# Optimization experiments

Measured on AMD Instinct MI355X. Metric: run time of the kernel, lower is better.

The kernel has to match this reference:

```python
import jax, jax.numpy as jnp
import numpy as np

NUM_HEADS = 12
WINDOW = 14
GLOBAL_LAYERS = (1,)
N_LAYERS = 2
EPS = 1e-6
PATCH = 16


def layer_norm(x, w, b):
    m = x.mean(-1, keepdims=True)
    v = ((x - m) ** 2).mean(-1, keepdims=True)
    return (x - m) * jax.lax.rsqrt(v + EPS) * w + b


def layer_norm_2d(x, w, b):
    # channels_first LayerNorm over C of [B,C,H,W]
    m = x.mean(1, keepdims=True)
    v = ((x - m) ** 2).mean(1, keepdims=True)
    return (x - m) * jax.lax.rsqrt(v + EPS) * w[None, :, None, None] + b[None, :, None, None]


def get_rel_pos(size, rel_pos):
    # q_size == k_size == size and rel_pos has exactly 2*size-1 rows,
    # so F.interpolate is identity -> direct relative-coordinate lookup.
    coords = jnp.arange(size)
    idx = coords[:, None] - coords[None, :] + (size - 1)  # [size, size]
    return rel_pos[idx]  # [size, size, head_dim]


def attention(x, qkv_w, qkv_b, proj_w, proj_b, rel_h, rel_w):
    B, H, W, C = x.shape
    hd = C // NUM_HEADS
    qkv = x.reshape(B, H * W, C) @ qkv_w.T + qkv_b                       # [B,HW,3C]
    qkv = qkv.reshape(B, H * W, 3, NUM_HEADS, hd).transpose(2, 0, 3, 1, 4)
    qkv = qkv.reshape(3, B * NUM_HEADS, H * W, hd)
    q, k, v = qkv[0], qkv[1], qkv[2]
    attn = jnp.einsum('bqd,bkd->bqk', q * (hd ** -0.5), k)               # [Bn,HW,HW]
    Rh = get_rel_pos(H, rel_h)                                           # [H,H,hd]
    Rw = get_rel_pos(W, rel_w)                                           # [W,W,hd]
    qr = q.reshape(B * NUM_HEADS, H, W, hd)
    rel_h_t = jnp.einsum('bhwc,hkc->bhwk', qr, Rh)                       # [Bn,H,W,H]
    rel_w_t = jnp.einsum('bhwc,wkc->bhwk', qr, Rw)                       # [Bn,H,W,W]
    attn = attn.reshape(B * NUM_HEADS, H, W, H, W)
    attn = attn + rel_h_t[:, :, :, :, None] + rel_w_t[:, :, :, None, :]
    attn = attn.reshape(B * NUM_HEADS, H * W, H * W)
    attn = jax.nn.softmax(attn.astype(jnp.float32), axis=-1).astype(q.dtype)
    out = jnp.einsum('bqk,bkd->bqd', attn, v)
    out = out.reshape(B, NUM_HEADS, H, W, hd).transpose(0, 2, 3, 1, 4).reshape(B, H, W, C)
    return out @ proj_w.T + proj_b


def window_partition(x, ws):
    B, H, W, C = x.shape
    pad_h = (-H) % ws
    pad_w = (-W) % ws
    x = jnp.pad(x, ((0, 0), (0, pad_h), (0, pad_w), (0, 0)))
    Hp, Wp = H + pad_h, W + pad_w
    x = x.reshape(B, Hp // ws, ws, Wp // ws, ws, C).transpose(0, 1, 3, 2, 4, 5)
    return x.reshape(-1, ws, ws, C), (Hp, Wp)


def window_unpartition(win, ws, pad_hw, hw):
    Hp, Wp = pad_hw
    H, W = hw
    C = win.shape[-1]
    B = win.shape[0] // ((Hp // ws) * (Wp // ws))
    x = win.reshape(B, Hp // ws, Wp // ws, ws, ws, C).transpose(0, 1, 3, 2, 4, 5)
    return x.reshape(B, Hp, Wp, C)[:, :H, :W, :]


def _forward(pixel_values, patch_w, patch_b, pos_embed, ln1_w, ln1_b, qkv_w, qkv_b,
             proj_w, proj_b, rel_h0, rel_w0, rel_h1, rel_w1, ln2_w, ln2_b,
             mlp1_w, mlp1_b, mlp2_w, mlp2_b, neck_conv1_w, neck_ln1_w, neck_ln1_b,
             neck_conv2_w, neck_ln2_w, neck_ln2_b):
    # patch embed (16x16 stride-16 conv) -> [B,64,64,768]
    x = jax.lax.conv_general_dilated(pixel_values, patch_w, (PATCH, PATCH), 'VALID',
                                     dimension_numbers=('NCHW', 'OIHW', 'NCHW'))
    x = x.transpose(0, 2, 3, 1) + patch_b
    x = x + pos_embed
    rels = [(rel_h0, rel_w0), (rel_h1, rel_w1)]
    for i in range(N_LAYERS):
        shortcut = x
        h = layer_norm(x, ln1_w[i], ln1_b[i])
        ws = 0 if i in GLOBAL_LAYERS else WINDOW
        if ws > 0:
            H, W = h.shape[1], h.shape[2]
            h, pad_hw = window_partition(h, ws)
        h = attention(h, qkv_w[i], qkv_b[i], proj_w[i], proj_b[i], *rels[i])
        if ws > 0:
            h = window_unpartition(h, ws, pad_hw, (H, W))
        x = shortcut + h
        m = layer_norm(x, ln2_w[i], ln2_b[i])
        m = jax.nn.gelu(m @ mlp1_w[i].T + mlp1_b[i], approximate=False)
        x = x + (m @ mlp2_w[i].T + mlp2_b[i])
    # neck: 1x1 conv -> LN2d -> 3x3 conv -> LN2d (convs have no bias)
    x = x.transpose(0, 3, 1, 2)                                          # [B,C,H,W]
    x = jnp.einsum('bchw,oc->bohw', x, neck_conv1_w[:, :, 0, 0])
    x = layer_norm_2d(x, neck_ln1_w, neck_ln1_b)
    x = jax.lax.conv_general_dilated(x, neck_conv2_w, (1, 1), ((1, 1), (1, 1)),
                                     dimension_numbers=('NCHW', 'OIHW', 'NCHW'))
    x = layer_norm_2d(x, neck_ln2_w, neck_ln2_b)
    return x


def setup_inputs() -> dict:
    ks = iter(jax.random.split(jax.random.key(0), 40))

    def rn(shape, s=0.02):
        return jax.random.normal(next(ks), shape, jnp.float32) * s

    C, NL, MLP, OC = 768, N_LAYERS, 3072, 256
    return {
        'pixel_values': jax.random.normal(next(ks), (1, 3, 1024, 1024), jnp.float32),
        'patch_w': rn((C, 3, PATCH, PATCH)),
        'patch_b': rn((C,)),
        'pos_embed': rn((1, 64, 64, C)),
        'ln1_w': jnp.ones((NL, C)), 'ln1_b': jnp.zeros((NL, C)),
        'qkv_w': rn((NL, 3 * C, C)), 'qkv_b': rn((NL, 3 * C)),
        'proj_w': rn((NL, C, C)), 'proj_b': rn((NL, C)),
        'rel_h0': rn((2 * WINDOW - 1, 64)), 'rel_w0': rn((2 * WINDOW - 1, 64)),
        'rel_h1': rn((2 * 64 - 1, 64)), 'rel_w1': rn((2 * 64 - 1, 64)),
        'ln2_w': jnp.ones((NL, C)), 'ln2_b': jnp.zeros((NL, C)),
        'mlp1_w': rn((NL, MLP, C)), 'mlp1_b': rn((NL, MLP)),
        'mlp2_w': rn((NL, C, MLP)), 'mlp2_b': rn((NL, C)),
        'neck_conv1_w': rn((OC, C, 1, 1)),
        'neck_ln1_w': jnp.ones((OC,)), 'neck_ln1_b': jnp.zeros((OC,)),
        'neck_conv2_w': rn((OC, OC, 3, 3)),
        'neck_ln2_w': jnp.ones((OC,)), 'neck_ln2_b': jnp.zeros((OC,)),
    }


def reference(pixel_values, patch_w, patch_b, pos_embed, ln1_w, ln1_b, qkv_w, qkv_b,
              proj_w, proj_b, rel_h0, rel_w0, rel_h1, rel_w1, ln2_w, ln2_b,
              mlp1_w, mlp1_b, mlp2_w, mlp2_b, neck_conv1_w, neck_ln1_w, neck_ln1_b,
              neck_conv2_w, neck_ln2_w, neck_ln2_b):
    return _forward(pixel_values, patch_w, patch_b, pos_embed, ln1_w, ln1_b, qkv_w,
                    qkv_b, proj_w, proj_b, rel_h0, rel_w0, rel_h1, rel_w1, ln2_w,
                    ln2_b, mlp1_w, mlp1_b, mlp2_w, mlp2_b, neck_conv1_w, neck_ln1_w,
                    neck_ln1_b, neck_conv2_w, neck_ln2_w, neck_ln2_b)
```

## Files before the change

kernel.cpp:

```cpp
#include <hip/hip_runtime.h>
#include <hip/hip_bf16.h>
#include <cmath>
#include <cstddef>

#define THREADS 256
typedef unsigned short u16;
typedef unsigned int u32;
typedef __attribute__((ext_vector_type(8))) short bf16x8;
typedef __attribute__((ext_vector_type(4))) float f32x4;
#define MFMA16(a, b, c) __builtin_amdgcn_mfma_f32_16x16x32_bf16(a, b, c, 0, 0, 0)

__device__ __forceinline__ float bf2f(u16 u) {
  union { u32 i; float f; } x; x.i = ((u32)u) << 16; return x.f;
}
__device__ __forceinline__ u16 f2bf(float f) {
  __hip_bfloat16 h = __float2bfloat16(f);
  return *reinterpret_cast<u16*>(&h);
}
__device__ __forceinline__ u32 f2bf2(float a, float b) {
  __hip_bfloat162 h = __float22bfloat162_rn(make_float2(a, b));
  return *reinterpret_cast<u32*>(&h);
}

__device__ __forceinline__ void gload16(const u16* g, u16* l) {
  __builtin_amdgcn_global_load_lds(
      (const __attribute__((address_space(1))) unsigned int*)g,
      (__attribute__((address_space(3))) unsigned int*)l, 16, 0, 0);
}

__device__ __forceinline__ float block_reduce_sum256(float v, float* red4) {
  for (int off = 32; off > 0; off >>= 1) v += __shfl_down(v, off);
  __syncthreads();
  if ((threadIdx.x & 63) == 0) red4[threadIdx.x >> 6] = v;
  __syncthreads();
  return red4[0] + red4[1] + red4[2] + red4[3];
}

__global__ void f2b_kernel(const float* __restrict__ in, u16* __restrict__ out,
                           int n) {
  int i = (blockIdx.x * THREADS + threadIdx.x) * 4;
  if (i >= n) return;
  float4 v = *reinterpret_cast<const float4*>(in + i);
  ushort4 o;
  o.x = f2bf(v.x); o.y = f2bf(v.y); o.z = f2bf(v.z); o.w = f2bf(v.w);
  *reinterpret_cast<ushort4*>(out + i) = o;
}

__global__ void neck2w_kernel(const float* __restrict__ src,
                              u16* __restrict__ dst) {
  int idx = blockIdx.x * THREADS + threadIdx.x;
  if (idx >= 256 * 2304) return;
  int o = idx / 2304, r = idx % 2304;
  int n9 = r >> 8, c = r & 255;
  dst[idx] = f2bf(src[(size_t)(o * 256 + c) * 9 + n9]);
}

__global__ void im2col_patch_kernel(const float* __restrict__ img,
                                    u16* __restrict__ out) {
  int idx = blockIdx.x * THREADS + threadIdx.x;
  if (idx >= 4096 * 768) return;
  int col = idx % 768, tok = idx / 768;
  int ph = tok / 64, pw = tok % 64;
  int c = col / 256, r = col % 256;
  int i = r / 16, j = r % 16;
  out[idx] = f2bf(img[(size_t)(c * 1024 + ph * 16 + i) * 1024 + pw * 16 + j]);
}

template <int MODE, int BN>
__global__ __launch_bounds__(256)
void gemm_bf16(const u16* __restrict__ A, const u16* __restrict__ B,
               const float* __restrict__ bias, const float* __restrict__ res,
               void* __restrict__ out, void* __restrict__ out2,
               int M, int N, int K) {
  constexpr int NF = BN / 32;
  __shared__ __attribute__((aligned(16))) u16 As[128 * 64];
  __shared__ __attribute__((aligned(16))) u16 Bs[BN * 64];
  const int t = threadIdx.x;
  const int w = t >> 6, l = t & 63;
  const int m0 = blockIdx.y * 128, n0 = blockIdx.x * BN;
  const int wm = (w >> 1) * 64, wn = (w & 1) * (BN / 2);
  f32x4 acc[4][NF];
#pragma unroll
  for (int i = 0; i < 4; ++i)
#pragma unroll
    for (int j = 0; j < NF; ++j) acc[i][j] = (f32x4){0.f, 0.f, 0.f, 0.f};

  const int rr = l >> 3;
  const int cc = ((l & 7) ^ rr) * 8;
  const u16* aP[4];
  const u16* bP[NF];
#pragma unroll
  for (int j = 0; j < 4; ++j) {
    int ar = m0 + w * 32 + j * 8 + rr;
    if (ar >= M) ar = M - 1;
    aP[j] = A + (size_t)ar * K + cc;
  }
#pragma unroll
  for (int j = 0; j < NF; ++j)
    bP[j] = B + (size_t)(n0 + w * (BN / 4) + j * 8 + rr) * K + cc;
  u16* asw = &As[w * 2048];
  u16* bsw = &Bs[w * (BN * 16)];

  for (int k0 = 0; k0 < K; k0 += 64) {
    __syncthreads();
#pragma unroll
    for (int j = 0; j < 4; ++j) gload16(aP[j] + k0, asw + j * 512);
#pragma unroll
    for (int j = 0; j < NF; ++j) gload16(bP[j] + k0, bsw + j * 512);
    asm volatile("s_waitcnt vmcnt(0)" ::: "memory");
    __syncthreads();
#pragma unroll
    for (int kc = 0; kc < 2; ++kc) {
      bf16x8 af[4], bf[NF];
#pragma unroll
      for (int i = 0; i < 4; ++i) {
        int ar = wm + i * 16 + (l & 15);
        int ac = (kc * 4 + (l >> 4)) ^ (ar & 7);
        af[i] = *reinterpret_cast<const bf16x8*>(&As[ar * 64 + ac * 8]);
      }
#pragma unroll
      for (int j = 0; j < NF; ++j) {
        int br = wn + j * 16 + (l & 15);
        int bc = (kc * 4 + (l >> 4)) ^ (br & 7);
        bf[j] = *reinterpret_cast<const bf16x8*>(&Bs[br * 64 + bc * 8]);
      }
#pragma unroll
      for (int i = 0; i < 4; ++i)
#pragma unroll
        for (int j = 0; j < NF; ++j)
          acc[i][j] = MFMA16(af[i], bf[j], acc[i][j]);
    }
  }

#pragma unroll
  for (int i = 0; i < 4; ++i) {
#pragma unroll
    for (int reg = 0; reg < 4; ++reg) {
      int m = m0 + wm + i * 16 + (l >> 4) * 4 + reg;
      if (m >= M) continue;
#pragma unroll
      for (int j = 0; j < NF; ++j) {
        int n = n0 + wn + j * 16 + (l & 15);
        float v = acc[i][j][reg];
        if (bias) v += bias[n];
        if (MODE == 0 || MODE == 3) {
          if (res) v += res[(size_t)m * N + n];
          ((float*)out)[(size_t)m * N + n] = v;
          if (MODE == 3) ((u16*)out2)[(size_t)m * N + n] = f2bf(v);
        } else if (MODE == 1) {
          v = 0.5f * v * (1.0f + erff(v * 0.70710678118654752f));
          ((u16*)out)[(size_t)m * N + n] = f2bf(v);
        } else {
          float sc = (n < 768) ? 0.125f : 1.0f;
          ((u16*)out)[(size_t)m * N + n] = f2bf(v * sc);
        }
      }
    }
  }
}

template <int WHICH>
__global__ __launch_bounds__(256)
void relpos_mfma_kernel(const u16* __restrict__ qkvb,
                        const u16* __restrict__ Rtab,
                        u16* __restrict__ relout) {
  __shared__ __attribute__((aligned(16))) u16 Ql[64 * 64];
  __shared__ __attribute__((aligned(16))) u16 Rl[64 * 64];
  const int t = threadIdx.x, w = t >> 6, l = t & 63;
  const int head = blockIdx.x >> 6;
  const int fixed = blockIdx.x & 63;
  const int rr = l >> 3;
  const int cc = ((l & 7) ^ rr) * 8;

#pragma unroll
  for (int j = 0; j < 2; ++j) {
    int row = w * 16 + j * 8 + rr;
    int tok = (WHICH == 0) ? (fixed * 64 + row) : (row * 64 + fixed);
    gload16(qkvb + (size_t)tok * 2304 + head * 64 + cc, &Ql[w * 1024 + j * 512]);
    int rrow = fixed - row + 63;
    gload16(Rtab + rrow * 64 + cc, &Rl[w * 1024 + j * 512]);
  }
  asm volatile("s_waitcnt vmcnt(0)" ::: "memory");
  __syncthreads();

  f32x4 acc[4];
#pragma unroll
  for (int j = 0; j < 4; ++j) acc[j] = (f32x4){0.f, 0.f, 0.f, 0.f};
#pragma unroll
  for (int kc = 0; kc < 2; ++kc) {
    int ar = w * 16 + (l & 15);
    int ac = (kc * 4 + (l >> 4)) ^ (ar & 7);
    bf16x8 af = *reinterpret_cast<const bf16x8*>(&Ql[ar * 64 + ac * 8]);
#pragma unroll
    for (int j = 0; j < 4; ++j) {
      int br = j * 16 + (l & 15);
      int bc = (kc * 4 + (l >> 4)) ^ (br & 7);
      bf16x8 bf = *reinterpret_cast<const bf16x8*>(&Rl[br * 64 + bc * 8]);
      acc[j] = MFMA16(af, bf, acc[j]);
    }
  }

#pragma unroll
  for (int j = 0; j < 4; ++j) {
#pragma unroll
    for (int reg = 0; reg < 4; ++reg) {
      int m = w * 16 + (l >> 4) * 4 + reg;
      int n = j * 16 + (l & 15);
      size_t o = (WHICH == 0)
                     ? ((((size_t)head * 64 + fixed) * 64 + m) * 64 + n)
                     : ((((size_t)head * 64 + m) * 64 + fixed) * 64 + n);
      relout[o] = f2bf(acc[j][reg] * 8.0f);
    }
  }
}

__global__ void ln_row_kernel(const float* __restrict__ in,
                              const float* __restrict__ w,
                              const float* __restrict__ b,
                              u16* __restrict__ out, int D) {
  __shared__ float red[4];
  size_t base = (size_t)blockIdx.x * D;
  float s = 0.f, s2 = 0.f;
  for (int i = threadIdx.x; i < D; i += THREADS) {
    float v = in[base + i];
    s += v; s2 += v * v;
  }
  s = block_reduce_sum256(s, red);
  s2 = block_reduce_sum256(s2, red);
  float m = s / (float)D;
  float var = s2 / (float)D - m * m;
  float inv = rsqrtf(var + 1e-6f);
  for (int i = threadIdx.x; i < D; i += THREADS) {
    float v = in[base + i];
    out[base + i] = f2bf((v - m) * inv * w[i] + b[i]);
  }
}

__global__ void win_part_kernel(const u16* __restrict__ h,
                                u16* __restrict__ out) {
  int idx = blockIdx.x * THREADS + threadIdx.x;
  if (idx >= 4900 * 768) return;
  int c = idx % 768;
  int tok = idx / 768;
  int win = tok / 196, r = tok % 196;
  int wy = r / 14, wx = r % 14;
  int gy = (win / 5) * 14 + wy;
  int gx = (win % 5) * 14 + wx;
  out[idx] = (gy < 64 && gx < 64) ? h[((size_t)gy * 64 + gx) * 768 + c] : (u16)0;
}

__global__ void win_unpart_add_kernel(const float* __restrict__ p,
                                      float* __restrict__ x) {
  int idx = blockIdx.x * THREADS + threadIdx.x;
  if (idx >= 4096 * 768) return;
  int c = idx % 768;
  int tok = idx / 768;
  int gy = tok / 64, gx = tok % 64;
  int win = (gy / 14) * 5 + (gx / 14);
  int wy = gy % 14, wx = gx % 14;
  x[idx] += p[((size_t)(win * 196 + wy * 14 + wx)) * 768 + c];
}

__global__ void add_kernel(const float* __restrict__ p, float* __restrict__ x,
                           int n) {
  int idx = blockIdx.x * THREADS + threadIdx.x;
  if (idx < n) x[idx] += p[idx];
}

__global__ void relpos_kernel(const u16* __restrict__ qkvb,
                              const float* __restrict__ rh_tab,
                              const float* __restrict__ rw_tab,
                              u16* __restrict__ relh,
                              u16* __restrict__ relw,
                              int S, int total) {
  int idx = blockIdx.x * THREADS + threadIdx.x;
  if (idx >= total) return;
  int k = idx % S;
  int r = idx / S;
  int qw = r % S; r /= S;
  int qh = r % S; r /= S;
  int head = r % 12;
  int win = r / 12;
  int seq = S * S;
  int tok = win * seq + qh * S + qw;
  const u16* q = qkvb + (size_t)tok * 2304 + head * 64;
  const float* rh = rh_tab + (size_t)(qh - k + S - 1) * 64;
  const float* rw = rw_tab + (size_t)(qw - k + S - 1) * 64;
  float sh = 0.f, sw = 0.f;
#pragma unroll
  for (int d0 = 0; d0 < 64; d0 += 8) {
    uint4 qv = *reinterpret_cast<const uint4*>(q + d0);
    u16 qs[8];
    *reinterpret_cast<uint4*>(qs) = qv;
#pragma unroll
    for (int i = 0; i < 8; ++i) {
      float qq = bf2f(qs[i]);
      sh = fmaf(qq, rh[d0 + i], sh);
      sw = fmaf(qq, rw[d0 + i], sw);
    }
  }
  relh[idx] = f2bf(sh * 8.0f);
  relw[idx] = f2bf(sw * 8.0f);
}

template <int S>
__global__ __launch_bounds__(256)
void attn_mfma_kernel(const u16* __restrict__ qkvb,
                      const u16* __restrict__ RHt,
                      const u16* __restrict__ RWt,
                      u16* __restrict__ out) {
  constexpr int SEQ = S * S;
  constexpr int NKT = (SEQ + 63) / 64;
  constexpr bool DB = (S == 64);
  constexpr int BIAS_N = (S == 14) ? 320 : 1024;
  extern __shared__ __attribute__((aligned(16))) u16 smem[];
  u16* KlA[2];
  u16* VtA[2];
  u16* Plb;
  u16* RHlb;
  u16* RWlb = nullptr;
  if constexpr (DB) {
    KlA[0] = smem;          KlA[1] = smem + 4096;
    VtA[0] = smem + 8192;   VtA[1] = smem + 12288;
    Plb = smem + 16384;
    RHlb = smem + 20480;
  } else {
    KlA[0] = smem;          KlA[1] = smem;
    VtA[0] = smem + 4096;   VtA[1] = smem + 4096;
    Plb = smem + 8192;
    RHlb = smem + 12288;
    RWlb = RHlb + 4 * BIAS_N;
  }

  const int t = threadIdx.x;
  const int w = t >> 6;
  const int l = t & 63;
  const int g = l >> 4;
  const int q = l & 15;
  const int bn = blockIdx.y;
  const int win = bn / 12, head = bn % 12;
  const int qbase = blockIdx.x * 64 + w * 16;
  const size_t tokbase = (size_t)win * SEQ;
  u16* Pl = Plb + w * 1024;
  u16* RHl = RHlb + w * BIAS_N;
  u16* RWl = RWlb + w * BIAS_N;

  {
    int ql = l >> 2;
    int qglob = qbase + ql;
    if (qglob > SEQ - 1) qglob = SEQ - 1;
    int qh = qglob / S, qw = qglob - qh * S;
    size_t bh = (((size_t)bn * S + qh) * S + qw) * S;
    for (int i = l & 3; i < S; i += 4) {
      RHl[i * 16 + ql] = RHt[bh + i];
      if constexpr (S == 14) RWl[i * 16 + ql] = RWt[bh + i];
    }
  }

  float rwreg[4][4];
  if constexpr (S == 64) {
    int qglob = qbase + q;
    size_t rwb = (((size_t)bn * 64 + (qglob >> 6)) * 64 + (qglob & 63)) * 64;
#pragma unroll
    for (int sub = 0; sub < 4; ++sub)
#pragma unroll
      for (int reg = 0; reg < 4; ++reg)
        rwreg[sub][reg] = bf2f(RWt[rwb + sub * 16 + g * 4 + reg]);
  }

  bf16x8 qf[2];
  {
    int qglob = qbase + q;
    if (qglob > SEQ - 1) qglob = SEQ - 1;
    const u16* qp = qkvb + (tokbase + qglob) * 2304 + head * 64 + g * 8;
    qf[0] = *reinterpret_cast<const bf16x8*>(qp);
    qf[1] = *reinterpret_cast<const bf16x8*>(qp + 32);
  }

  float m_run = -1e30f, l_run = 0.f;
  f32x4 Oacc[4];
#pragma unroll
  for (int dn = 0; dn < 4; ++dn) Oacc[dn] = (f32x4){0.f, 0.f, 0.f, 0.f};

  const int rr = l >> 3;
  const int kcc = ((l & 7) ^ rr) * 8;
  const int vkey = t & 63, vdg = t >> 6;

  auto stageK = [&](int kt, u16* Kd) {
#pragma unroll
    for (int j = 0; j < 2; ++j) {
      int kk = kt * 64 + w * 16 + j * 8 + rr;
      if (kk > SEQ - 1) kk = SEQ - 1;
      gload16(qkvb + (tokbase + kk) * 2304 + 768 + head * 64 + kcc,
              &Kd[w * 1024 + j * 512]);
    }
  };
  auto loadV = [&](int kt, uint4& a, uint4& b) {
    int kk = kt * 64 + vkey;
    if (kk > SEQ - 1) kk = SEQ - 1;
    const uint4* src = reinterpret_cast<const uint4*>(
        qkvb + (tokbase + kk) * 2304 + 1536 + head * 64 + vdg * 16);
    a = src[0];
    b = src[1];
  };
  auto writeV = [&](uint4 a, uint4 b, u16* Vd) {
    u16 arr[16];
    *reinterpret_cast<uint4*>(&arr[0]) = a;
    *reinterpret_cast<uint4*>(&arr[8]) = b;
#pragma unroll
    for (int i = 0; i < 16; ++i)
      Vd[(vdg * 16 + i) * 64 + (vkey ^ ((i & 7) << 3))] = arr[i];
  };

  auto computeTile = [&](int kt, u16* Kl, u16* Vt) {
    const int k0 = kt * 64;
    f32x4 Sacc[4];
#pragma unroll
    for (int sub = 0; sub < 4; ++sub) {
      Sacc[sub] = (f32x4){0.f, 0.f, 0.f, 0.f};
#pragma unroll
      for (int kc = 0; kc < 2; ++kc) {
        int key = sub * 16 + q;
        int chunk = (kc * 4 + g) ^ (key & 7);
        bf16x8 kfr = *reinterpret_cast<const bf16x8*>(&Kl[key * 64 + (chunk << 3)]);
        Sacc[sub] = MFMA16(kfr, qf[kc], Sacc[sub]);
      }
    }

    float sv[4][4];
    float tmax = -1e30f;
    if constexpr (S == 64) {
      float rhv = bf2f(RHl[kt * 16 + q]);
#pragma unroll
      for (int sub = 0; sub < 4; ++sub)
#pragma unroll
        for (int reg = 0; reg < 4; ++reg) {
          float s = Sacc[sub][reg] + rhv + rwreg[sub][reg];
          sv[sub][reg] = s;
          tmax = fmaxf(tmax, s);
        }
    } else {
#pragma unroll
      for (int sub = 0; sub < 4; ++sub)
#pragma unroll
        for (int reg = 0; reg < 4; ++reg) {
          int key = k0 + sub * 16 + g * 4 + reg;
          float s = -1e30f;
          if (key < SEQ) {
            int kh = key / S, kw = key - kh * S;
            s = Sacc[sub][reg] + bf2f(RHl[kh * 16 + q]) + bf2f(RWl[kw * 16 + q]);
          }
          sv[sub][reg] = s;
          tmax = fmaxf(tmax, s);
        }
    }
    tmax = fmaxf(tmax, __shfl_xor(tmax, 16));
    tmax = fmaxf(tmax, __shfl_xor(tmax, 32));

    if (!__all(tmax - m_run <= 8.0f)) {
      float mn = fmaxf(m_run, tmax);
      float sc = __expf(m_run - mn);
      l_run *= sc;
      m_run = mn;
#pragma unroll
      for (int reg = 0; reg < 4; ++reg) {
        float scq = __shfl(sc, g * 4 + reg);
#pragma unroll
        for (int dn = 0; dn < 4; ++dn) Oacc[dn][reg] *= scq;
      }
    }

    float psum = 0.f;
#pragma unroll
    for (int sub = 0; sub < 4; ++sub)
#pragma unroll
      for (int pr = 0; pr < 2; ++pr) {
        float p0 = __expf(sv[sub][2 * pr] - m_run);
        float p1 = __expf(sv[sub][2 * pr + 1] - m_run);
        psum += p0 + p1;
        u32 pk = f2bf2(p0, p1);
        int idx = (q * 64 + sub * 16 + g * 4 + pr * 2) ^ ((q & 7) << 3);
        *reinterpret_cast<u32*>(&Pl[idx]) = pk;
      }
    psum += __shfl_xor(psum, 16);
    psum += __shfl_xor(psum, 32);
    l_run += psum;

#pragma unroll
    for (int kc = 0; kc < 2; ++kc) {
      int chunk = (kc * 4 + g) ^ (q & 7);
      bf16x8 pa = *reinterpret_cast<const bf16x8*>(&Pl[q * 64 + (chunk << 3)]);
#pragma unroll
      for (int dn = 0; dn < 4; ++dn) {
        bf16x8 vb = *reinterpret_cast<const bf16x8*>(
            &Vt[(dn * 16 + q) * 64 + (chunk << 3)]);
        Oacc[dn] = MFMA16(pa, vb, Oacc[dn]);
      }
    }
  };

  if constexpr (DB) {
    uint4 va, vb0;
    stageK(0, KlA[0]);
    loadV(0, va, vb0);
    asm volatile("s_waitcnt vmcnt(0)" ::: "memory");
    writeV(va, vb0, VtA[0]);
    __syncthreads();
    for (int kt = 0; kt < NKT; ++kt) {
      const int cur = kt & 1;
      const bool pf = (kt + 1 < NKT);
      if (pf) {
        stageK(kt + 1, KlA[cur ^ 1]);
        loadV(kt + 1, va, vb0);
      }
      computeTile(kt, KlA[cur], VtA[cur]);
      if (pf) {
        asm volatile("s_waitcnt vmcnt(0)" ::: "memory");
        writeV(va, vb0, VtA[cur ^ 1]);
      }
      __syncthreads();
    }
  } else {
    for (int kt = 0; kt < NKT; ++kt) {
      __syncthreads();
      stageK(kt, KlA[0]);
      uint4 va, vb0;
      loadV(kt, va, vb0);
      writeV(va, vb0, VtA[0]);
      asm volatile("s_waitcnt vmcnt(0)" ::: "memory");
      __syncthreads();
      computeTile(kt, KlA[0], VtA[0]);
    }
  }

  float invq = 1.0f / l_run;
#pragma unroll
  for (int reg = 0; reg < 4; ++reg) {
    int ql = g * 4 + reg;
    int qglob = qbase + ql;
    if (qglob >= SEQ) continue;
    float inv = __shfl(invq, ql);
    u16* op = out + (tokbase + qglob) * 768 + head * 64;
#pragma unroll
    for (int dn = 0; dn < 4; ++dn)
      op[dn * 16 + q] = f2bf(Oacc[dn][reg] * inv);
  }
}

__global__ void neck_im2col_kernel(const u16* __restrict__ ln,
                                   u16* __restrict__ out) {
  int idx = blockIdx.x * THREADS + threadIdx.x;
  if (idx >= 4096 * 2304) return;
  int col = idx % 2304, tok = idx / 2304;
  int n9 = col >> 8, c = col & 255;
  int y = tok >> 6, x = tok & 63;
  int yy = y + n9 / 3 - 1, xx = x + n9 % 3 - 1;
  out[idx] = (yy >= 0 && yy < 64 && xx >= 0 && xx < 64)
                 ? ln[((size_t)yy * 64 + xx) * 256 + c]
                 : (u16)0;
}

__global__ void ln2d_out_kernel(const float* __restrict__ in,
                                const float* __restrict__ w,
                                const float* __restrict__ b,
                                float* __restrict__ out) {
  __shared__ float red[4];
  int tok = blockIdx.x, t = threadIdx.x;
  float v = in[(size_t)tok * 256 + t];
  float s = block_reduce_sum256(v, red);
  float m = s / 256.f;
  float dv = v - m;
  float s2 = block_reduce_sum256(dv * dv, red);
  float inv = rsqrtf(s2 / 256.f + 1e-6f);
  out[(size_t)t * 4096 + tok] = dv * inv * w[t] + b[t];
}

extern "C" void kernel_launch(void* const* d_in, const int* in_sizes, int n_in,
                              void* d_out, int out_size, void* d_ws,
                              size_t ws_size, hipStream_t stream) {
  const float* pixel_values = (const float*)d_in[0];
  const float* patch_w = (const float*)d_in[1];
  const float* patch_b = (const float*)d_in[2];
  const float* pos_embed = (const float*)d_in[3];
  const float* ln1_w = (const float*)d_in[4];
  const float* ln1_b = (const float*)d_in[5];
  const float* qkv_w = (const float*)d_in[6];
  const float* qkv_b = (const float*)d_in[7];
  const float* proj_w = (const float*)d_in[8];
  const float* proj_b = (const float*)d_in[9];
  const float* rel_h0 = (const float*)d_in[10];
  const float* rel_w0 = (const float*)d_in[11];
  const float* rel_h1 = (const float*)d_in[12];
  const float* rel_w1 = (const float*)d_in[13];
  const float* ln2_w = (const float*)d_in[14];
  const float* ln2_b = (const float*)d_in[15];
  const float* mlp1_w = (const float*)d_in[16];
  const float* mlp1_b = (const float*)d_in[17];
  const float* mlp2_w = (const float*)d_in[18];
  const float* mlp2_b = (const float*)d_in[19];
  const float* neck1_w = (const float*)d_in[20];
  const float* nln1_w = (const float*)d_in[21];
  const float* nln1_b = (const float*)d_in[22];
  const float* neck2_w = (const float*)d_in[23];
  const float* nln2_w = (const float*)d_in[24];
  const float* nln2_b = (const float*)d_in[25];
  float* out = (float*)d_out;

  float* X = (float*)d_ws;
  u16* Xb = (u16*)(X + 3145728);
  float* H = (float*)(Xb + 3145728);
  u16* Ab1 = (u16*)(H + 3763200);
  u16* Ab2 = Ab1 + 3763200;
  u16* QKVb = Ab2 + 12582912;
  u16* RHb = QKVb + 11289600;
  u16* RWb = RHb + 3145728;
  u16* AOb = RWb + 3145728;
  u16* Wb = AOb + 3763200;
  u16* RTb = Wb + 2359296;
  u16* RTb2 = RTb + 8128;
  u16* LNb = Ab2 + 11520000;

#define CVT(src, n) f2b_kernel<<<((n) / 4 + THREADS - 1) / THREADS, THREADS, 0, stream>>>(src, Wb, n)

  im2col_patch_kernel<<<12288, THREADS, 0, stream>>>(pixel_values, Ab2);
  CVT(patch_w, 589824);
  gemm_bf16<0, 64><<<dim3(12, 32), THREADS, 0, stream>>>(
      Ab2, Wb, patch_b, pos_embed, X, nullptr, 4096, 768, 768);

  ln_row_kernel<<<4096, THREADS, 0, stream>>>(X, ln1_w, ln1_b, Ab2, 768);
  win_part_kernel<<<14700, THREADS, 0, stream>>>(Ab2, Ab1);
  CVT(qkv_w, 1769472);
  gemm_bf16<2, 128><<<dim3(18, 39), THREADS, 0, stream>>>(
      Ab1, Wb, qkv_b, nullptr, QKVb, nullptr, 4900, 2304, 768);
  {
    int total = 25 * 12 * 14 * 14 * 14;
    relpos_kernel<<<(total + THREADS - 1) / THREADS, THREADS, 0, stream>>>(
        QKVb, rel_h0, rel_w0, RHb, RWb, 14, total);
  }
  attn_mfma_kernel<14><<<dim3(4, 300), THREADS, 29696, stream>>>(QKVb, RHb, RWb, AOb);
  CVT(proj_w, 589824);
  gemm_bf16<0, 64><<<dim3(12, 39), THREADS, 0, stream>>>(
      AOb, Wb, proj_b, nullptr, H, nullptr, 4900, 768, 768);
  win_unpart_add_kernel<<<12288, THREADS, 0, stream>>>(H, X);
  ln_row_kernel<<<4096, THREADS, 0, stream>>>(X, ln2_w, ln2_b, Ab1, 768);
  CVT(mlp1_w, 2359296);
  gemm_bf16<1, 128><<<dim3(24, 32), THREADS, 0, stream>>>(
      Ab1, Wb, mlp1_b, nullptr, Ab2, nullptr, 4096, 3072, 768);
  CVT(mlp2_w, 2359296);
  gemm_bf16<0, 64><<<dim3(12, 32), THREADS, 0, stream>>>(
      Ab2, Wb, mlp2_b, X, X, nullptr, 4096, 768, 3072);

  ln_row_kernel<<<4096, THREADS, 0, stream>>>(X, ln1_w + 768, ln1_b + 768, Ab1, 768);
  CVT(qkv_w + (size_t)2304 * 768, 1769472);
  gemm_bf16<2, 128><<<dim3(18, 32), THREADS, 0, stream>>>(
      Ab1, Wb, qkv_b + 2304, nullptr, QKVb, nullptr, 4096, 2304, 768);
  f2b_kernel<<<8, THREADS, 0, stream>>>(rel_h1, RTb, 8128);
  f2b_kernel<<<8, THREADS, 0, stream>>>(rel_w1, RTb2, 8128);
  relpos_mfma_kernel<0><<<768, THREADS, 0, stream>>>(QKVb, RTb, RHb);
  relpos_mfma_kernel<1><<<768, THREADS, 0, stream>>>(QKVb, RTb2, RWb);
  attn_mfma_kernel<64><<<dim3(64, 12), THREADS, 49152, stream>>>(QKVb, RHb, RWb, AOb);
  CVT(proj_w + (size_t)768 * 768, 589824);
  gemm_bf16<0, 64><<<dim3(12, 32), THREADS, 0, stream>>>(
      AOb, Wb, proj_b + 768, nullptr, H, nullptr, 4096, 768, 768);
  add_kernel<<<12288, THREADS, 0, stream>>>(H, X, 4096 * 768);
  ln_row_kernel<<<4096, THREADS, 0, stream>>>(X, ln2_w + 768, ln2_b + 768, Ab1, 768);
  CVT(mlp1_w + (size_t)3072 * 768, 2359296);
  gemm_bf16<1, 128><<<dim3(24, 32), THREADS, 0, stream>>>(
      Ab1, Wb, mlp1_b + 3072, nullptr, Ab2, nullptr, 4096, 3072, 768);
  CVT(mlp2_w + (size_t)768 * 3072, 2359296);
  gemm_bf16<3, 64><<<dim3(12, 32), THREADS, 0, stream>>>(
      Ab2, Wb, mlp2_b + 768, X, X, Xb, 4096, 768, 3072);

  CVT(neck1_w, 196608);
  gemm_bf16<0, 64><<<dim3(4, 32), THREADS, 0, stream>>>(
      Xb, Wb, nullptr, nullptr, H, nullptr, 4096, 256, 768);
  ln_row_kernel<<<4096, THREADS, 0, stream>>>(H, nln1_w, nln1_b, LNb, 256);
  neck2w_kernel<<<2304, THREADS, 0, stream>>>(neck2_w, Wb);
  neck_im2col_kernel<<<36864, THREADS, 0, stream>>>(LNb, Ab2);
  gemm_bf16<0, 64><<<dim3(4, 32), THREADS, 0, stream>>>(
      Ab2, Wb, nullptr, nullptr, H, nullptr, 4096, 256, 2304);
  ln2d_out_kernel<<<4096, THREADS, 0, stream>>>(H, nln2_w, nln2_b, out);
}
```

Before: 1.030 ms.

## Fold rel-pos table conversion into relpos kernel and stage two KV tiles per sync

The relpos MFMA kernel now reads the fp32 rel-pos tables directly and converts them to bf16 in registers while writing LDS. This drops the two separate f2b conversion launches. The global attention kernel replaces its register-prefetched double buffer with a scheme that loads two K/V tiles together, then computes both. That halves barrier count but removes the overlap of the next tile's loads with compute. The bf16 LDS write order for the rel-pos table must match the swizzled layout that gload16 produced, and the pairing assumes NKT is even (64 tiles).

```diff
diff --git a/kernel.cpp b/kernel.cpp
--- a/kernel.cpp
+++ b/kernel.cpp
@@ -20,6 +20,10 @@
 __device__ __forceinline__ u32 f2bf2(float a, float b) {
   __hip_bfloat162 h = __float22bfloat162_rn(make_float2(a, b));
   return *reinterpret_cast<u32*>(&h);
+}
+__device__ __forceinline__ uint4 cvt8(float4 x0, float4 x1) {
+  return make_uint4(f2bf2(x0.x, x0.y), f2bf2(x0.z, x0.w),
+                    f2bf2(x1.x, x1.y), f2bf2(x1.z, x1.w));
 }
 
 __device__ __forceinline__ void gload16(const u16* g, u16* l) {
@@ -162,7 +166,7 @@
 template <int WHICH>
 __global__ __launch_bounds__(256)
 void relpos_mfma_kernel(const u16* __restrict__ qkvb,
-                        const u16* __restrict__ Rtab,
+                        const float* __restrict__ Rtab,
                         u16* __restrict__ relout) {
   __shared__ __attribute__((aligned(16))) u16 Ql[64 * 64];
   __shared__ __attribute__((aligned(16))) u16 Rl[64 * 64];
@@ -178,7 +182,10 @@
     int tok = (WHICH == 0) ? (fixed * 64 + row) : (row * 64 + fixed);
     gload16(qkvb + (size_t)tok * 2304 + head * 64 + cc, &Ql[w * 1024 + j * 512]);
     int rrow = fixed - row + 63;
-    gload16(Rtab + rrow * 64 + cc, &Rl[w * 1024 + j * 512]);
+    const float* rs = Rtab + (size_t)rrow * 64 + cc;
+    float4 x0 = *reinterpret_cast<const float4*>(rs);
+    float4 x1 = *reinterpret_cast<const float4*>(rs + 4);
+    *reinterpret_cast<uint4*>(&Rl[w * 1024 + j * 512 + l * 8]) = cvt8(x0, x1);
   }
   asm volatile("s_waitcnt vmcnt(0)" ::: "memory");
   __syncthreads();
@@ -311,22 +318,18 @@
                       u16* __restrict__ out) {
   constexpr int SEQ = S * S;
   constexpr int NKT = (SEQ + 63) / 64;
-  constexpr bool DB = (S == 64);
+  constexpr bool TWO = (S == 64);
   constexpr int BIAS_N = (S == 14) ? 320 : 1024;
   extern __shared__ __attribute__((aligned(16))) u16 smem[];
-  u16* KlA[2];
-  u16* VtA[2];
-  u16* Plb;
-  u16* RHlb;
-  u16* RWlb = nullptr;
-  if constexpr (DB) {
-    KlA[0] = smem;          KlA[1] = smem + 4096;
-    VtA[0] = smem + 8192;   VtA[1] = smem + 12288;
+  u16 *Kl0, *Kl1, *Vt0, *Vt1, *Plb, *RHlb, *RWlb = nullptr;
+  if constexpr (TWO) {
+    Kl0 = smem;          Kl1 = smem + 4096;
+    Vt0 = smem + 8192;   Vt1 = smem + 12288;
     Plb = smem + 16384;
     RHlb = smem + 20480;
   } else {
-    KlA[0] = smem;          KlA[1] = smem;
-    VtA[0] = smem + 4096;   VtA[1] = smem + 4096;
+    Kl0 = smem;          Kl1 = smem;
+    Vt0 = smem + 4096;   Vt1 = smem + 4096;
     Plb = smem + 8192;
     RHlb = smem + 12288;
     RWlb = RHlb + 4 * BIAS_N;
@@ -395,15 +398,12 @@
               &Kd[w * 1024 + j * 512]);
     }
   };
-  auto loadV = [&](int kt, uint4& a, uint4& b) {
+  auto stageV = [&](int kt, u16* Vd) {
     int kk = kt * 64 + vkey;
     if (kk > SEQ - 1) kk = SEQ - 1;
     const uint4* src = reinterpret_cast<const uint4*>(
         qkvb + (tokbase + kk) * 2304 + 1536 + head * 64 + vdg * 16);
-    a = src[0];
-    b = src[1];
-  };
-  auto writeV = [&](uint4 a, uint4 b, u16* Vd) {
+    uint4 a = src[0], b = src[1];
     u16 arr[16];
     *reinterpret_cast<uint4*>(&arr[0]) = a;
     *reinterpret_cast<uint4*>(&arr[8]) = b;
@@ -499,37 +499,26 @@
     }
   };
 
-  if constexpr (DB) {
-    uint4 va, vb0;
-    stageK(0, KlA[0]);
-    loadV(0, va, vb0);
-    asm volatile("s_waitcnt vmcnt(0)" ::: "memory");
-    writeV(va, vb0, VtA[0]);
-    __syncthreads();
-    for (int kt = 0; kt < NKT; ++kt) {
-      const int cur = kt & 1;
-      const bool pf = (kt + 1 < NKT);
-      if (pf) {
-        stageK(kt + 1, KlA[cur ^ 1]);
-        loadV(kt + 1, va, vb0);
-      }
-      computeTile(kt, KlA[cur], VtA[cur]);
-      if (pf) {
-        asm volatile("s_waitcnt vmcnt(0)" ::: "memory");
-        writeV(va, vb0, VtA[cur ^ 1]);
-      }
+  if constexpr (TWO) {
+    for (int kt = 0; kt < NKT; kt += 2) {
       __syncthreads();
+      stageK(kt, Kl0);
+      stageK(kt + 1, Kl1);
+      stageV(kt, Vt0);
+      stageV(kt + 1, Vt1);
+      asm volatile("s_waitcnt vmcnt(0)" ::: "memory");
+      __syncthreads();
+      computeTile(kt, Kl0, Vt0);
+      computeTile(kt + 1, Kl1, Vt1);
     }
   } else {
     for (int kt = 0; kt < NKT; ++kt) {
       __syncthreads();
-      stageK(kt, KlA[0]);
-      uint4 va, vb0;
-      loadV(kt, va, vb0);
-      writeV(va, vb0, VtA[0]);
+      stageK(kt, Kl0);
+      stageV(kt, Vt0);
       asm volatile("s_waitcnt vmcnt(0)" ::: "memory");
       __syncthreads();
-      computeTile(kt, KlA[0], VtA[0]);
+      computeTile(kt, Kl0, Vt0);
     }
   }
 
@@ -616,8 +605,6 @@
   u16* RWb = RHb + 3145728;
   u16* AOb = RWb + 3145728;
   u16* Wb = AOb + 3763200;
-  u16* RTb = Wb + 2359296;
-  u16* RTb2 = RTb + 8128;
   u16* LNb = Ab2 + 11520000;
 
 #define CVT(src, n) f2b_kernel<<<((n) / 4 + THREADS - 1) / THREADS, THREADS, 0, stream>>>(src, Wb, n)
@@ -654,10 +641,8 @@
   CVT(qkv_w + (size_t)2304 * 768, 1769472);
   gemm_bf16<2, 128><<<dim3(18, 32), THREADS, 0, stream>>>(
       Ab1, Wb, qkv_b + 2304, nullptr, QKVb, nullptr, 4096, 2304, 768);
-  f2b_kernel<<<8, THREADS, 0, stream>>>(rel_h1, RTb, 8128);
-  f2b_kernel<<<8, THREADS, 0, stream>>>(rel_w1, RTb2, 8128);
-  relpos_mfma_kernel<0><<<768, THREADS, 0, stream>>>(QKVb, RTb, RHb);
-  relpos_mfma_kernel<1><<<768, THREADS, 0, stream>>>(QKVb, RTb2, RWb);
+  relpos_mfma_kernel<0><<<768, THREADS, 0, stream>>>(QKVb, rel_h1, RHb);
+  relpos_mfma_kernel<1><<<768, THREADS, 0, stream>>>(QKVb, rel_w1, RWb);
   attn_mfma_kernel<64><<<dim3(64, 12), THREADS, 49152, stream>>>(QKVb, RHb, RWb, AOb);
   CVT(proj_w + (size_t)768 * 768, 589824);
   gemm_bf16<0, 64><<<dim3(12, 32), THREADS, 0, stream>>>(
```

Result: faster. 984.6 us (-4.4%).
